# Kernel tuning notes

Measured on AMD Instinct MI355X. Metric: run time of the kernel, lower is better.

## Reference

```python
import jax, jax.numpy as jnp
import numpy as np

N_NODES = 50000
N_EDGES = 800000
D_IN = 128
D_OUT = 128
N_GRAPHS = 512
N_CONVS = 5
EPS = 1e-5


def setup_inputs() -> dict:
    key = jax.random.key(0)
    ks = jax.random.split(key, 8)
    x = jax.random.normal(ks[0], (N_NODES, D_IN), dtype=jnp.float32)
    edge_index = jax.random.randint(ks[1], (2, N_EDGES), 0, N_NODES, dtype=jnp.int32)
    batch = jnp.sort(jax.random.randint(ks[2], (N_NODES,), 0, N_GRAPHS, dtype=jnp.int32))
    s = 1.0 / np.sqrt(D_IN)
    W_rel = jax.random.normal(ks[3], (N_CONVS, D_OUT, D_IN), dtype=jnp.float32) * s
    b_rel = jax.random.normal(ks[4], (N_CONVS, D_OUT), dtype=jnp.float32) * s
    W_root = jax.random.normal(ks[5], (N_CONVS, D_OUT, D_IN), dtype=jnp.float32) * s
    gamma = jnp.ones((D_OUT,), dtype=jnp.float32)
    beta = jnp.zeros((D_OUT,), dtype=jnp.float32)
    Wc = jax.random.normal(ks[6], (96, D_OUT), dtype=jnp.float32) * (1.0 / np.sqrt(D_OUT))
    bc = jax.random.normal(ks[7], (96,), dtype=jnp.float32) * (1.0 / np.sqrt(D_OUT))
    return {"x": x, "edge_index": edge_index, "batch": batch, "i": 0,
            "W_rel": W_rel, "b_rel": b_rel, "W_root": W_root,
            "gamma": gamma, "beta": beta, "Wc": Wc, "bc": bc}


def reference(x, edge_index, batch, i, W_rel, b_rel, W_root, gamma, beta, Wc, bc):
    # --- 5 GraphConv branches, summed. GraphConv: lin_rel(sum_{j->i} x_j) + lin_root(x).
    # Sum over the 5 convs commutes with the linears, so fold the weights first.
    src, dst = edge_index[0], edge_index[1]
    agg = jax.ops.segment_sum(x[src], dst, num_segments=N_NODES)  # [N, D_in]
    Wr = jnp.sum(W_rel, axis=0)   # [D_out, D_in]
    Wt = jnp.sum(W_root, axis=0)  # [D_out, D_in]
    br = jnp.sum(b_rel, axis=0)   # [D_out]
    h = agg @ Wr.T + x @ Wt.T + br  # [N, D_out]
    # --- NodeLevelBatchNorm (training: batch stats over all nodes, biased var)
    mean = jnp.mean(h, axis=0)
    var = jnp.mean((h - mean) ** 2, axis=0)
    h = gamma * (h - mean) * jax.lax.rsqrt(var + EPS) + beta
    # --- global max pool over graphs, relu, classifier (i=0 -> no-dropout branch)
    pooled = jax.ops.segment_max(h, batch, num_segments=N_GRAPHS)  # [G, D_out]
    pooled = jax.nn.relu(pooled)
    return pooled @ Wc.T + bc  # [G, 96]
```

## Files before the change

kernel.cpp:

```cpp
#include <hip/hip_runtime.h>

#define EPS 1e-5f

constexpr int NN = 50000, NE = 800000, DD = 128, NG = 512, NC = 5, NO = 96;
constexpr int MAXB = 8192;
constexpr int NBUCK = 196;

typedef __attribute__((ext_vector_type(8))) short bf16x8;
typedef __attribute__((ext_vector_type(4))) float f32x4;

constexpr size_t HB   = 0;
constexpr size_t XB   = (size_t)NN * DD / 2;
constexpr size_t WB   = XB + (size_t)NN * DD / 2;
constexpr size_t BRO  = WB + DD * 256 / 2;
constexpr size_t CSUM = BRO + DD;
constexpr size_t CSQ  = CSUM + DD;
constexpr size_t POOL = CSQ + DD;
constexpr size_t GCNT = POOL + (size_t)NG * DD;
constexpr size_t ZEND = GCNT + 256;
constexpr size_t ROFF = ZEND;
constexpr size_t BSTOR= ROFF + NN + 1;
constexpr size_t CSR16= BSTOR + (size_t)NBUCK*MAXB;

constexpr int XCAST_B = NN * DD / 4 / 256;
constexpr int FOLD_B  = DD * DD / 256;
constexpr int BUCK_B  = (NE + 4095) / 4096;

static __device__ __forceinline__ unsigned short f2b(float f) {
    unsigned int u = __float_as_uint(f);
    return (unsigned short)((u + 0x7FFFu + ((u >> 16) & 1u)) >> 16);
}
static __device__ __forceinline__ float b2f(unsigned short h) {
    return __uint_as_float(((unsigned int)h) << 16);
}
static __device__ __forceinline__ unsigned fkey(float f) {
    unsigned u = __float_as_uint(f);
    return (u >> 31) ? ~u : (u | 0x80000000u);
}
static __device__ __forceinline__ float unfkey(unsigned k) {
    unsigned u = (k & 0x80000000u) ? (k ^ 0x80000000u) : ~k;
    return __uint_as_float(u);
}

__global__ __launch_bounds__(256) void k_prep(const float* __restrict__ x,
                                              const float* __restrict__ Wrel,
                                              const float* __restrict__ brel,
                                              const float* __restrict__ Wroot,
                                              const int* __restrict__ ei,
                                              float* __restrict__ ws, int* __restrict__ wi) {
    __shared__ int lcnt[256];
    __shared__ int lbase[256];
    int b = blockIdx.x, t = threadIdx.x;
    if (b < XCAST_B) {
        int i = b * 256 + t;
        float4 v = ((const float4*)x)[i];
        ushort4 o = {f2b(v.x), f2b(v.y), f2b(v.z), f2b(v.w)};
        ((ushort4*)(ws + XB))[i] = o;
    } else if (b < XCAST_B + FOLD_B) {
        int idx = (b - XCAST_B) * 256 + t;
        int k = idx >> 7, o = idx & 127;
        float wr = 0.f, wt = 0.f;
        for (int c = 0; c < NC; ++c) {
            wr += Wrel [c*DD*DD + o*DD + k];
            wt += Wroot[c*DD*DD + o*DD + k];
        }
        unsigned short* wb = (unsigned short*)(ws + WB);
        wb[o*256 + k]       = f2b(wr);
        wb[o*256 + 128 + k] = f2b(wt);
        if (k == 0) {
            float bias = 0.f;
            for (int c = 0; c < NC; ++c) bias += brel[c*DD + o];
            ws[BRO + o] = bias;
        }
    } else {
        int bb = b - XCAST_B - FOLD_B;
        lcnt[t] = 0;
        __syncthreads();
        int val[16], krk[16];
        #pragma unroll
        for (int j = 0; j < 16; ++j) {
            int e = bb * 4096 + j * 256 + t;
            krk[j] = -1;
            if (e < NE) {
                int d = ei[NE + e], s = ei[e];
                int key = d >> 8;
                int r = atomicAdd(&lcnt[key], 1);
                val[j] = s | ((d & 255) << 16);
                krk[j] = (key << 16) | r;
            }
        }
        __syncthreads();
        if (t < NBUCK && lcnt[t] > 0)
            lbase[t] = atomicAdd(&wi[GCNT + t], lcnt[t]);
        __syncthreads();
        #pragma unroll
        for (int j = 0; j < 16; ++j) {
            if (krk[j] >= 0) {
                int key = krk[j] >> 16, r = krk[j] & 0xFFFF;
                int p = lbase[key] + r;
                if (p < MAXB) wi[BSTOR + (size_t)key * MAXB + p] = val[j];
            }
        }
    }
}

__global__ __launch_bounds__(256) void k_sort(int* __restrict__ wi) {
    __shared__ int eds[MAXB];
    __shared__ unsigned short srt[MAXB];
    __shared__ int cnt[256], cnt2[256], lscan[256], gall[256];
    int t = threadIdx.x, b = blockIdx.x;
    int g = wi[GCNT + t];
    gall[t] = g; lscan[t] = g; cnt[t] = 0;
    __syncthreads();
    for (int off = 1; off < 256; off <<= 1) {
        int u = (t >= off) ? gall[t - off] : 0;
        __syncthreads();
        gall[t] += u;
        __syncthreads();
    }
    int base = gall[b] - lscan[b];
    int C = lscan[b]; if (C > MAXB) C = MAXB;
    __syncthreads();
    for (int i = t; i < C; i += 256) {
        int v = wi[BSTOR + (size_t)b * MAXB + i];
        eds[i] = v;
        atomicAdd(&cnt[v >> 16], 1);
    }
    __syncthreads();
    int cv = cnt[t];
    for (int off = 1; off < 256; off <<= 1) {
        int u = (t >= off) ? cnt[t - off] : 0;
        __syncthreads();
        cnt[t] += u;
        __syncthreads();
    }
    lscan[t] = cnt[t] - cv;
    cnt2[t] = 0;
    __syncthreads();
    int n = b * 256 + t;
    if (n < NN) wi[ROFF + n] = base + lscan[t];
    if (b == 0 && t == 0) wi[ROFF + NN] = NE;
    for (int i = t; i < C; i += 256) {
        int v = eds[i], k = v >> 16;
        int p = lscan[k] + atomicAdd(&cnt2[k], 1);
        srt[p] = (unsigned short)(v & 0xFFFF);
    }
    __syncthreads();
    unsigned short* csr = (unsigned short*)(wi + CSR16);
    for (int i = t; i < C; i += 256)
        csr[base + i] = srt[i];
}

__global__ __launch_bounds__(256) void k_gg(const int* __restrict__ batch,
                                            const int* __restrict__ wi,
                                            float* __restrict__ ws) {
    __shared__ __align__(16) unsigned short aggS[32 * 128];
    __shared__ int batchS[32];
    __shared__ unsigned maxS[4][128];
    const unsigned short* xb  = (const unsigned short*)(ws + XB);
    const unsigned short* wbp = (const unsigned short*)(ws + WB);
    const unsigned short* csr = (const unsigned short*)(wi + CSR16);
    unsigned* poolU = (unsigned*)(ws + POOL);
    int tid = threadIdx.x;
    int row0g = blockIdx.x * 32;

    for (int i = tid; i < 4 * 128; i += 256) ((unsigned*)maxS)[i] = 0u;
    if (tid < 32) {
        int r = row0g + tid; if (r > NN - 1) r = NN - 1;
        batchS[tid] = batch[r];
    }

    {
        int sub = tid & 15, c8 = sub * 8;
        for (int round = 0; round < 2; ++round) {
            int row = round * 16 + (tid >> 4);
            int n = row0g + row;
            float acc[8] = {};
            if (n < NN) {
                int e0 = wi[ROFF + n], e1 = wi[ROFF + n + 1];
                int cnt = e1 - e0;
                int base = 0;
                for (; base + 16 <= cnt; base += 16) {
                    int myE = (int)csr[e0 + base + sub];
                    #pragma unroll
                    for (int j = 0; j < 16; ++j) {
                        int s = __shfl(myE, j, 16);
                        bf16x8 v = *(const bf16x8*)&xb[(size_t)s * DD + c8];
                        #pragma unroll
                        for (int c = 0; c < 8; ++c) acc[c] += b2f((unsigned short)v[c]);
                    }
                }
                int rem = cnt - base;
                if (rem > 0) {
                    int myE = (sub < rem) ? (int)csr[e0 + base + sub] : 0;
                    for (int j = 0; j < rem; ++j) {
                        int s = __shfl(myE, j, 16);
                        bf16x8 v = *(const bf16x8*)&xb[(size_t)s * DD + c8];
                        #pragma unroll
                        for (int c = 0; c < 8; ++c) acc[c] += b2f((unsigned short)v[c]);
                    }
                }
            }
            bf16x8 o;
            #pragma unroll
            for (int c = 0; c < 8; ++c) o[c] = (short)f2b(acc[c]);
            *(bf16x8*)((char*)aggS + row * 256 + ((sub * 16) ^ ((row & 7) << 4))) = o;
        }
    }
    __syncthreads();

    int wave = tid >> 6, lane = tid & 63;
    int quad = lane >> 4, l16 = lane & 15;
    int cw = wave * 32;
    int gBase = batchS[0];
    float bias[2] = { ws[BRO + cw + l16], ws[BRO + cw + 16 + l16] };
    f32x4 acc[2][2] = {};
    #pragma unroll
    for (int rt = 0; rt < 2; ++rt) {
        int row = rt * 16 + l16;
        int arow = row0g + row; if (arow > NN - 1) arow = NN - 1;
        const unsigned short* xRow = xb + (size_t)arow * DD;
        bf16x8 af[8];
        #pragma unroll
        for (int kt = 0; kt < 4; ++kt)
            af[kt] = *(const bf16x8*)((const char*)aggS + row * 256 +
                                      ((kt * 64 + quad * 16) ^ ((row & 7) << 4)));
        #pragma unroll
        for (int kt = 4; kt < 8; ++kt)
            af[kt] = *(const bf16x8*)(xRow + (kt - 4) * 32 + quad * 8);
        #pragma unroll
        for (int kt = 0; kt < 8; ++kt) {
            bf16x8 b0 = *(const bf16x8*)(wbp + (size_t)(cw + l16) * 256 + kt * 32 + quad * 8);
            bf16x8 b1 = *(const bf16x8*)(wbp + (size_t)(cw + 16 + l16) * 256 + kt * 32 + quad * 8);
            acc[rt][0] = __builtin_amdgcn_mfma_f32_16x16x32_bf16(af[kt], b0, acc[rt][0], 0, 0, 0);
            acc[rt][1] = __builtin_amdgcn_mfma_f32_16x16x32_bf16(af[kt], b1, acc[rt][1], 0, 0, 0);
        }
    }
    float csum[2] = {}, csq[2] = {};
    float mx[2]; int gcur = -1;
    #pragma unroll
    for (int rt = 0; rt < 2; ++rt) {
        #pragma unroll
        for (int r = 0; r < 4; ++r) {
            int lrow = rt * 16 + quad * 4 + r;
            int grow = row0g + lrow;
            if (grow < NN) {
                float v0 = acc[rt][0][r] + bias[0];
                float v1 = acc[rt][1][r] + bias[1];
                csum[0] += v0; csq[0] += v0 * v0;
                csum[1] += v1; csq[1] += v1 * v1;
                int g = batchS[lrow];
                if (g != gcur) {
                    if (gcur >= 0) {
                        int rel = gcur - gBase;
                        if (rel < 4) {
                            atomicMax(&maxS[rel][cw + l16], fkey(mx[0]));
                            atomicMax(&maxS[rel][cw + 16 + l16], fkey(mx[1]));
                        } else {
                            atomicMax(&poolU[(size_t)gcur * DD + cw + l16], fkey(mx[0]));
                            atomicMax(&poolU[(size_t)gcur * DD + cw + 16 + l16], fkey(mx[1]));
                        }
                    }
                    gcur = g; mx[0] = v0; mx[1] = v1;
                } else {
                    mx[0] = fmaxf(mx[0], v0); mx[1] = fmaxf(mx[1], v1);
                }
            }
        }
    }
    if (gcur >= 0) {
        int rel = gcur - gBase;
        if (rel < 4) {
            atomicMax(&maxS[rel][cw + l16], fkey(mx[0]));
            atomicMax(&maxS[rel][cw + 16 + l16], fkey(mx[1]));
        } else {
            atomicMax(&poolU[(size_t)gcur * DD + cw + l16], fkey(mx[0]));
            atomicMax(&poolU[(size_t)gcur * DD + cw + 16 + l16], fkey(mx[1]));
        }
    }
    #pragma unroll
    for (int ct = 0; ct < 2; ++ct) {
        float cs = csum[ct], cq = csq[ct];
        cs += __shfl_xor(cs, 16); cs += __shfl_xor(cs, 32);
        cq += __shfl_xor(cq, 16); cq += __shfl_xor(cq, 32);
        if (quad == 0) {
            atomicAdd(&ws[CSUM + cw + ct * 16 + l16], cs);
            atomicAdd(&ws[CSQ  + cw + ct * 16 + l16], cq);
        }
    }
    __syncthreads();
    int span = batchS[31] - gBase + 1; if (span > 4) span = 4;
    for (int i = tid; i < span * 128; i += 256) {
        unsigned k = ((unsigned*)maxS)[i];
        if (k) atomicMax(&poolU[(size_t)(gBase + (i >> 7)) * DD + (i & 127)], k);
    }
}

__global__ __launch_bounds__(128) void k_out(const float* __restrict__ gamma,
                                             const float* __restrict__ beta,
                                             const float* __restrict__ Wc,
                                             const float* __restrict__ bc,
                                             const float* __restrict__ ws,
                                             float* __restrict__ out) {
    __shared__ float pS[128];
    int g = blockIdx.x, t = threadIdx.x;
    float mean = ws[CSUM + t] * (1.0f / NN);
    float var  = ws[CSQ + t] * (1.0f / NN) - mean * mean;
    float sc   = gamma[t] * rsqrtf(var + EPS);
    float sh   = beta[t] - sc * mean;
    unsigned k = ((const unsigned*)(ws + POOL))[(size_t)g * DD + t];
    float p = 0.f;
    if (k) p = fmaxf(unfkey(k) * sc + sh, 0.f);
    pS[t] = p;
    __syncthreads();
    if (t < NO) {
        float acc = bc[t];
        #pragma unroll 8
        for (int kk = 0; kk < DD; ++kk) acc += pS[kk] * Wc[t*DD + kk];
        out[g*NO + t] = acc;
    }
}

extern "C" void kernel_launch(void* const* d_in, const int* in_sizes, int n_in,
                              void* d_out, int out_size, void* d_ws, size_t ws_size,
                              hipStream_t stream) {
    const float* x     = (const float*)d_in[0];
    const int*   ei    = (const int*)  d_in[1];
    const int*   batch = (const int*)  d_in[2];
    const float* Wrel  = (const float*)d_in[4];
    const float* brel  = (const float*)d_in[5];
    const float* Wroot = (const float*)d_in[6];
    const float* gamma = (const float*)d_in[7];
    const float* beta  = (const float*)d_in[8];
    const float* Wc    = (const float*)d_in[9];
    const float* bc    = (const float*)d_in[10];
    float* ws  = (float*)d_ws;
    int*   wi  = (int*)d_ws;
    float* out = (float*)d_out;

    hipMemsetAsync(ws + CSUM, 0, (ZEND - CSUM) * sizeof(float), stream);

    k_prep <<<XCAST_B + FOLD_B + BUCK_B, 256, 0, stream>>>(x, Wrel, brel, Wroot, ei, ws, wi);
    k_sort <<<NBUCK, 256, 0, stream>>>(wi);
    k_gg   <<<(NN + 31)/32, 256, 0, stream>>>(batch, wi, ws);
    k_out  <<<NG, 128, 0, stream>>>(gamma, beta, Wc, bc, ws, out);
}
```

Measured before the change: 201.8 us.

## Replace bucketed LDS sort with global histogram counting-sort CSR and split gather/GEMM

```diff
diff --git a/kernel.cpp b/kernel.cpp
--- a/kernel.cpp
+++ b/kernel.cpp
@@ -3,8 +3,7 @@
 #define EPS 1e-5f
 
 constexpr int NN = 50000, NE = 800000, DD = 128, NG = 512, NC = 5, NO = 96;
-constexpr int MAXB = 8192;
-constexpr int NBUCK = 196;
+constexpr int NBLK = (NN + 255) / 256;
 
 typedef __attribute__((ext_vector_type(8))) short bf16x8;
 typedef __attribute__((ext_vector_type(4))) float f32x4;
@@ -16,15 +15,17 @@
 constexpr size_t CSUM = BRO + DD;
 constexpr size_t CSQ  = CSUM + DD;
 constexpr size_t POOL = CSQ + DD;
-constexpr size_t GCNT = POOL + (size_t)NG * DD;
-constexpr size_t ZEND = GCNT + 256;
+constexpr size_t HIST = POOL + (size_t)NG * DD;
+constexpr size_t ZEND = HIST + NN;
 constexpr size_t ROFF = ZEND;
-constexpr size_t BSTOR= ROFF + NN + 1;
-constexpr size_t CSR16= BSTOR + (size_t)NBUCK*MAXB;
+constexpr size_t CUR  = ROFF + NN + 1;
+constexpr size_t GSUM = CUR + NN;
+constexpr size_t CSR16= GSUM + 256;
 
 constexpr int XCAST_B = NN * DD / 4 / 256;
 constexpr int FOLD_B  = DD * DD / 256;
-constexpr int BUCK_B  = (NE + 4095) / 4096;
+constexpr int HIST_B  = (NE + 2047) / 2048;
+constexpr int PLACE_B = (NE + 1023) / 1024;
 
 static __device__ __forceinline__ unsigned short f2b(float f) {
     unsigned int u = __float_as_uint(f);
@@ -48,8 +49,6 @@
                                               const float* __restrict__ Wroot,
                                               const int* __restrict__ ei,
                                               float* __restrict__ ws, int* __restrict__ wi) {
-    __shared__ int lcnt[256];
-    __shared__ int lbase[256];
     int b = blockIdx.x, t = threadIdx.x;
     if (b < XCAST_B) {
         int i = b * 256 + t;
@@ -74,141 +73,124 @@
         }
     } else {
         int bb = b - XCAST_B - FOLD_B;
-        lcnt[t] = 0;
+        #pragma unroll
+        for (int j = 0; j < 8; ++j) {
+            int e = bb * 2048 + j * 256 + t;
+            if (e < NE) atomicAdd(&wi[HIST + ei[NE + e]], 1);
+        }
+    }
+}
+
+__global__ __launch_bounds__(256) void k_scanA(int* __restrict__ wi) {
+    __shared__ int sc[256];
+    int t = threadIdx.x, b = blockIdx.x;
+    int n = b * 256 + t;
+    int h = (n < NN) ? wi[HIST + n] : 0;
+    sc[t] = h;
+    __syncthreads();
+    for (int off = 1; off < 256; off <<= 1) {
+        int u = (t >= off) ? sc[t - off] : 0;
         __syncthreads();
-        int val[16], krk[16];
+        sc[t] += u;
+        __syncthreads();
+    }
+    if (n < NN) wi[ROFF + n] = sc[t] - h;
+    if (t == 255) wi[GSUM + b] = sc[255];
+}
+
+__global__ __launch_bounds__(256) void k_fix(int* __restrict__ wi) {
+    __shared__ int sc[256], orig[256];
+    int t = threadIdx.x, b = blockIdx.x;
+    int g = (t < NBLK) ? wi[GSUM + t] : 0;
+    sc[t] = g; orig[t] = g;
+    __syncthreads();
+    for (int off = 1; off < 256; off <<= 1) {
+        int u = (t >= off) ? sc[t - off] : 0;
+        __syncthreads();
+        sc[t] += u;
+        __syncthreads();
+    }
+    int base = sc[b] - orig[b];
+    int n = b * 256 + t;
+    if (n < NN) {
+        int v = wi[ROFF + n] + base;
+        wi[ROFF + n] = v;
+        wi[CUR + n] = v;
+    }
+    if (b == 0 && t == 0) wi[ROFF + NN] = NE;
+}
+
+__global__ __launch_bounds__(256) void k_place(const int* __restrict__ ei,
+                                               int* __restrict__ wi) {
+    unsigned short* csr = (unsigned short*)(wi + CSR16);
+    int b = blockIdx.x, t = threadIdx.x;
+    #pragma unroll
+    for (int j = 0; j < 4; ++j) {
+        int e = b * 1024 + j * 256 + t;
+        if (e < NE) {
+            int d = ei[NE + e], s = ei[e];
+            int p = atomicAdd(&wi[CUR + d], 1);
+            csr[p] = (unsigned short)s;
+        }
+    }
+}
+
+__global__ __launch_bounds__(256) void k_gather(const int* __restrict__ wi,
+                                                float* __restrict__ ws) {
+    const unsigned short* xb = (const unsigned short*)(ws + XB);
+    const unsigned short* csr = (const unsigned short*)(wi + CSR16);
+    unsigned short* hb = (unsigned short*)(ws + HB);
+    int tid = threadIdx.x;
+    int n   = blockIdx.x * 16 + (tid >> 4);
+    int sub = tid & 15;
+    int c8  = sub * 8;
+    if (n >= NN) return;
+    int e0 = wi[ROFF + n], e1 = wi[ROFF + n + 1];
+    int cnt = e1 - e0;
+    float acc[8] = {};
+    int base = 0;
+    for (; base + 16 <= cnt; base += 16) {
+        int myE = (int)csr[e0 + base + sub];
         #pragma unroll
         for (int j = 0; j < 16; ++j) {
-            int e = bb * 4096 + j * 256 + t;
-            krk[j] = -1;
-            if (e < NE) {
-                int d = ei[NE + e], s = ei[e];
-                int key = d >> 8;
-                int r = atomicAdd(&lcnt[key], 1);
-                val[j] = s | ((d & 255) << 16);
-                krk[j] = (key << 16) | r;
-            }
-        }
-        __syncthreads();
-        if (t < NBUCK && lcnt[t] > 0)
-            lbase[t] = atomicAdd(&wi[GCNT + t], lcnt[t]);
-        __syncthreads();
-        #pragma unroll
-        for (int j = 0; j < 16; ++j) {
-            if (krk[j] >= 0) {
-                int key = krk[j] >> 16, r = krk[j] & 0xFFFF;
-                int p = lbase[key] + r;
-                if (p < MAXB) wi[BSTOR + (size_t)key * MAXB + p] = val[j];
-            }
-        }
-    }
-}
-
-__global__ __launch_bounds__(256) void k_sort(int* __restrict__ wi) {
-    __shared__ int eds[MAXB];
-    __shared__ unsigned short srt[MAXB];
-    __shared__ int cnt[256], cnt2[256], lscan[256], gall[256];
-    int t = threadIdx.x, b = blockIdx.x;
-    int g = wi[GCNT + t];
-    gall[t] = g; lscan[t] = g; cnt[t] = 0;
-    __syncthreads();
-    for (int off = 1; off < 256; off <<= 1) {
-        int u = (t >= off) ? gall[t - off] : 0;
-        __syncthreads();
-        gall[t] += u;
-        __syncthreads();
-    }
-    int base = gall[b] - lscan[b];
-    int C = lscan[b]; if (C > MAXB) C = MAXB;
-    __syncthreads();
-    for (int i = t; i < C; i += 256) {
-        int v = wi[BSTOR + (size_t)b * MAXB + i];
-        eds[i] = v;
-        atomicAdd(&cnt[v >> 16], 1);
-    }
-    __syncthreads();
-    int cv = cnt[t];
-    for (int off = 1; off < 256; off <<= 1) {
-        int u = (t >= off) ? cnt[t - off] : 0;
-        __syncthreads();
-        cnt[t] += u;
-        __syncthreads();
-    }
-    lscan[t] = cnt[t] - cv;
-    cnt2[t] = 0;
-    __syncthreads();
-    int n = b * 256 + t;
-    if (n < NN) wi[ROFF + n] = base + lscan[t];
-    if (b == 0 && t == 0) wi[ROFF + NN] = NE;
-    for (int i = t; i < C; i += 256) {
-        int v = eds[i], k = v >> 16;
-        int p = lscan[k] + atomicAdd(&cnt2[k], 1);
-        srt[p] = (unsigned short)(v & 0xFFFF);
-    }
-    __syncthreads();
-    unsigned short* csr = (unsigned short*)(wi + CSR16);
-    for (int i = t; i < C; i += 256)
-        csr[base + i] = srt[i];
-}
-
-__global__ __launch_bounds__(256) void k_gg(const int* __restrict__ batch,
-                                            const int* __restrict__ wi,
-                                            float* __restrict__ ws) {
-    __shared__ __align__(16) unsigned short aggS[32 * 128];
+            int s = __shfl(myE, j, 16);
+            bf16x8 v = *(const bf16x8*)&xb[(size_t)s * DD + c8];
+            #pragma unroll
+            for (int c = 0; c < 8; ++c) acc[c] += b2f((unsigned short)v[c]);
+        }
+    }
+    int rem = cnt - base;
+    if (rem > 0) {
+        int myE = (sub < rem) ? (int)csr[e0 + base + sub] : 0;
+        for (int j = 0; j < rem; ++j) {
+            int s = __shfl(myE, j, 16);
+            bf16x8 v = *(const bf16x8*)&xb[(size_t)s * DD + c8];
+            #pragma unroll
+            for (int c = 0; c < 8; ++c) acc[c] += b2f((unsigned short)v[c]);
+        }
+    }
+    bf16x8 o;
+    #pragma unroll
+    for (int c = 0; c < 8; ++c) o[c] = (short)f2b(acc[c]);
+    *(bf16x8*)&hb[(size_t)n * DD + c8] = o;
+}
+
+__global__ __launch_bounds__(256) void k_gemm(const int* __restrict__ batch,
+                                              float* __restrict__ ws) {
     __shared__ int batchS[32];
     __shared__ unsigned maxS[4][128];
+    const unsigned short* hb  = (const unsigned short*)(ws + HB);
     const unsigned short* xb  = (const unsigned short*)(ws + XB);
     const unsigned short* wbp = (const unsigned short*)(ws + WB);
-    const unsigned short* csr = (const unsigned short*)(wi + CSR16);
     unsigned* poolU = (unsigned*)(ws + POOL);
     int tid = threadIdx.x;
     int row0g = blockIdx.x * 32;
-
     for (int i = tid; i < 4 * 128; i += 256) ((unsigned*)maxS)[i] = 0u;
     if (tid < 32) {
         int r = row0g + tid; if (r > NN - 1) r = NN - 1;
         batchS[tid] = batch[r];
     }
-
-    {
-        int sub = tid & 15, c8 = sub * 8;
-        for (int round = 0; round < 2; ++round) {
-            int row = round * 16 + (tid >> 4);
-            int n = row0g + row;
-            float acc[8] = {};
-            if (n < NN) {
-                int e0 = wi[ROFF + n], e1 = wi[ROFF + n + 1];
-                int cnt = e1 - e0;
-                int base = 0;
-                for (; base + 16 <= cnt; base += 16) {
-                    int myE = (int)csr[e0 + base + sub];
-                    #pragma unroll
-                    for (int j = 0; j < 16; ++j) {
-                        int s = __shfl(myE, j, 16);
-                        bf16x8 v = *(const bf16x8*)&xb[(size_t)s * DD + c8];
-                        #pragma unroll
-                        for (int c = 0; c < 8; ++c) acc[c] += b2f((unsigned short)v[c]);
-                    }
-                }
-                int rem = cnt - base;
-                if (rem > 0) {
-                    int myE = (sub < rem) ? (int)csr[e0 + base + sub] : 0;
-                    for (int j = 0; j < rem; ++j) {
-                        int s = __shfl(myE, j, 16);
-                        bf16x8 v = *(const bf16x8*)&xb[(size_t)s * DD + c8];
-                        #pragma unroll
-                        for (int c = 0; c < 8; ++c) acc[c] += b2f((unsigned short)v[c]);
-                    }
-                }
-            }
-            bf16x8 o;
-            #pragma unroll
-            for (int c = 0; c < 8; ++c) o[c] = (short)f2b(acc[c]);
-            *(bf16x8*)((char*)aggS + row * 256 + ((sub * 16) ^ ((row & 7) << 4))) = o;
-        }
-    }
-    __syncthreads();
-
+    __syncthreads();
     int wave = tid >> 6, lane = tid & 63;
     int quad = lane >> 4, l16 = lane & 15;
     int cw = wave * 32;
@@ -217,21 +199,17 @@
     f32x4 acc[2][2] = {};
     #pragma unroll
     for (int rt = 0; rt < 2; ++rt) {
-        int row = rt * 16 + l16;
-        int arow = row0g + row; if (arow > NN - 1) arow = NN - 1;
-        const unsigned short* xRow = xb + (size_t)arow * DD;
+        int arow = row0g + rt * 16 + l16; if (arow > NN - 1) arow = NN - 1;
+        const unsigned short* aggRow = hb + (size_t)arow * DD;
+        const unsigned short* xRow   = xb + (size_t)arow * DD;
         bf16x8 af[8];
         #pragma unroll
-        for (int kt = 0; kt < 4; ++kt)
-            af[kt] = *(const bf16x8*)((const char*)aggS + row * 256 +
-                                      ((kt * 64 + quad * 16) ^ ((row & 7) << 4)));
-        #pragma unroll
-        for (int kt = 4; kt < 8; ++kt)
-            af[kt] = *(const bf16x8*)(xRow + (kt - 4) * 32 + quad * 8);
+        for (int kt = 0; kt < 8; ++kt)
+            af[kt] = *(const bf16x8*)((kt < 4 ? aggRow + kt*32 : xRow + (kt-4)*32) + quad*8);
         #pragma unroll
         for (int kt = 0; kt < 8; ++kt) {
-            bf16x8 b0 = *(const bf16x8*)(wbp + (size_t)(cw + l16) * 256 + kt * 32 + quad * 8);
-            bf16x8 b1 = *(const bf16x8*)(wbp + (size_t)(cw + 16 + l16) * 256 + kt * 32 + quad * 8);
+            bf16x8 b0 = *(const bf16x8*)(wbp + (size_t)(cw + l16) * 256 + kt*32 + quad*8);
+            bf16x8 b1 = *(const bf16x8*)(wbp + (size_t)(cw + 16 + l16) * 256 + kt*32 + quad*8);
             acc[rt][0] = __builtin_amdgcn_mfma_f32_16x16x32_bf16(af[kt], b0, acc[rt][0], 0, 0, 0);
             acc[rt][1] = __builtin_amdgcn_mfma_f32_16x16x32_bf16(af[kt], b1, acc[rt][1], 0, 0, 0);
         }
@@ -340,8 +318,11 @@
 
     hipMemsetAsync(ws + CSUM, 0, (ZEND - CSUM) * sizeof(float), stream);
 
-    k_prep <<<XCAST_B + FOLD_B + BUCK_B, 256, 0, stream>>>(x, Wrel, brel, Wroot, ei, ws, wi);
-    k_sort <<<NBUCK, 256, 0, stream>>>(wi);
-    k_gg   <<<(NN + 31)/32, 256, 0, stream>>>(batch, wi, ws);
-    k_out  <<<NG, 128, 0, stream>>>(gamma, beta, Wc, bc, ws, out);
-}
+    k_prep  <<<XCAST_B + FOLD_B + HIST_B, 256, 0, stream>>>(x, Wrel, brel, Wroot, ei, ws, wi);
+    k_scanA <<<NBLK, 256, 0, stream>>>(wi);
+    k_fix   <<<NBLK, 256, 0, stream>>>(wi);
+    k_place <<<PLACE_B, 256, 0, stream>>>(ei, wi);
+    k_gather<<<(NN + 15)/16, 256, 0, stream>>>(wi, ws);
+    k_gemm  <<<(NN + 31)/32, 256, 0, stream>>>(batch, ws);
+    k_out   <<<NG, 128, 0, stream>>>(gamma, beta, Wc, bc, ws, out);
+}
```

Result: slower. 284.8 us (+41.1%).
